# Kernel optimization log

Hardware: AMD Instinct MI355X
Metric: run time of the kernel (lower is better)

## Reference

```python
import jax, jax.numpy as jnp
import numpy as np

B, TH, TS, HS, WS = 16, 1024, 1024, 1024, 1024


def setup_inputs() -> dict:
    key = jax.random.key(0)
    k1, k2, k3, k4 = jax.random.split(key, 4)
    h = jax.random.normal(k1, (B, TH, HS), dtype=jnp.float32)
    s = jax.random.normal(k2, (B, TS, WS), dtype=jnp.float32)
    # nn.Linear params: weight [out, in], bias [out]
    Wh = jax.random.normal(k3, (HS, HS), dtype=jnp.float32) * 0.02
    bh = jnp.zeros((HS,), dtype=jnp.float32)
    Ws = jax.random.normal(k4, (HS, WS), dtype=jnp.float32) * 0.02
    bs = jnp.zeros((HS,), dtype=jnp.float32)
    return {"h": h, "s": s, "Wh": Wh, "bh": bh, "Ws": Ws, "bs": bs}


def reference(h, s, Wh, bh, Ws, bs):
    hp = jnp.einsum('bth,oh->bto', h, Wh) + bh          # [B, TH, HS]
    sp = jnp.einsum('btw,ow->bto', s, Ws) + bs          # [B, TS, HS]
    scores = jnp.einsum('bik,bjk->bij', hp, sp)         # [B, TH, TS]
    b, th, _ = scores.shape
    # faithful to torch: flat-chunk into rows of length TH, softmax over dim 1
    sm = jax.nn.softmax(scores.reshape(-1, th), axis=1).reshape(b, -1, th)  # [B, TS, TH]
    res = jnp.matmul(sm, hp)                            # [B, TS, HS]
    return res.reshape(-1, res.shape[-1])               # [B*TS, HS]
```

## Files before the change

### kernel.cpp

```cpp
#include <hip/hip_runtime.h>
#include <hip/hip_bf16.h>
#include <stdint.h>


typedef _Float16 half_t;
typedef __attribute__((ext_vector_type(8))) _Float16 half8;
typedef __attribute__((ext_vector_type(4))) _Float16 half4;
typedef __attribute__((ext_vector_type(4))) float floatx4;

__device__ __forceinline__ void gl2lds16(const void* g, void* l) {
    __builtin_amdgcn_global_load_lds(
        (const __attribute__((address_space(1))) uint32_t*)(uintptr_t)g,
        (__attribute__((address_space(3))) uint32_t*)(uintptr_t)l,
        16, 0, 0);
}

template<int WH16T>
__global__ __launch_bounds__(256, 4) void gemm128(
    const half_t* __restrict__ A, const half_t* __restrict__ B,
    const float* __restrict__ bias,
    half_t* __restrict__ Ch, half_t* __restrict__ ChT)
{
    __shared__ char smem[32768];

    const int tid  = threadIdx.x;
    const int wave = tid >> 6;
    const int lane = tid & 63;
    const int wr = wave >> 1, wc = wave & 1;
    const int lr = lane & 15, lg = lane >> 4;

    const int row0 = blockIdx.x * 128;
    const int col0 = blockIdx.y * 128;

    floatx4 acc[4][4];
#pragma unroll
    for (int m = 0; m < 4; ++m)
#pragma unroll
        for (int n = 0; n < 4; ++n)
            acc[m][n] = (floatx4){0.f, 0.f, 0.f, 0.f};

    long aOff[2], bOff[2];
#pragma unroll
    for (int i = 0; i < 2; ++i) {
        const int off = i * 4096 + tid * 16;
        const int e = off ^ (((off >> 7) & 3) << 4);
        const int r = e >> 6, cb = e & 63;
        aOff[i] = (long)(row0 + r) * 2048 + cb;
        bOff[i] = (long)(col0 + r) * 2048 + cb;
    }
    const int wave_s = __builtin_amdgcn_readfirstlane(wave);

    auto stage = [&](int buf, int kk) {
#pragma unroll
        for (int i = 0; i < 2; ++i)
            gl2lds16((const char*)A + aOff[i] + (long)kk * 2,
                     smem + buf * 16384 + i * 4096 + wave_s * 1024);
#pragma unroll
        for (int i = 0; i < 2; ++i)
            gl2lds16((const char*)B + bOff[i] + (long)kk * 2,
                     smem + buf * 16384 + 8192 + i * 4096 + wave_s * 1024);
    };

    const uint32_t swx = (uint32_t)((lg * 16) ^ (((lr >> 1) & 3) << 4));
    uint32_t aof = (uint32_t)((wr * 64 + lr) * 64) + swx;
    uint32_t bof = 8192u + (uint32_t)((wc * 64 + lr) * 64) + swx;

    stage(0, 0);
    __syncthreads();

    for (int t = 0; t < 32; ++t) {
        if (t + 1 < 32) stage((t & 1) ^ 1, (t + 1) * 32);

        half8 aF[4], bF[4];
#pragma unroll
        for (int ni = 0; ni < 4; ++ni)
            bF[ni] = *(const half8*)(smem + bof + ni * 1024);
#pragma unroll
        for (int mi = 0; mi < 4; ++mi)
            aF[mi] = *(const half8*)(smem + aof + mi * 1024);
#pragma unroll
        for (int mi = 0; mi < 4; ++mi)
#pragma unroll
            for (int ni = 0; ni < 4; ++ni)
                acc[mi][ni] = __builtin_amdgcn_mfma_f32_16x16x32_f16(
                    aF[mi], bF[ni], acc[mi][ni], 0, 0, 0);

        __syncthreads();
        aof ^= 16384; bof ^= 16384;
    }

    {
        float* wlds = (float*)(smem + wave * 2304);
        float bv[4];
#pragma unroll
        for (int n = 0; n < 4; ++n)
            bv[n] = bias[col0 + wc * 64 + n * 16 + lr];
        const int er = lane >> 2, ec = lane & 3;
        const int oc = lane >> 1, tc = lane & 1;
#pragma unroll
        for (int m = 0; m < 4; ++m) {
#pragma unroll
            for (int np = 0; np < 2; ++np) {
#pragma unroll
                for (int n2 = 0; n2 < 2; ++n2)
#pragma unroll
                    for (int j = 0; j < 4; ++j)
                        wlds[(lg * 4 + j) * 36 + n2 * 16 + lr] =
                            acc[m][np * 2 + n2][j] + bv[np * 2 + n2];
                const int grow = row0 + wr * 64 + m * 16;
                const int gcol = col0 + wc * 64 + np * 32;
                float4 q0 = *(float4*)&wlds[er * 36 + ec * 8];
                float4 q1 = *(float4*)&wlds[er * 36 + ec * 8 + 4];
                {
                    half8 o = { (half_t)q0.x, (half_t)q0.y, (half_t)q0.z, (half_t)q0.w,
                                (half_t)q1.x, (half_t)q1.y, (half_t)q1.z, (half_t)q1.w };
                    *(half8*)&Ch[(long)(grow + er) * 1024 + gcol + ec * 8] = o;
                }
                if (WH16T) {
                    float tv[8];
#pragma unroll
                    for (int k = 0; k < 8; ++k)
                        tv[k] = wlds[(tc * 8 + k) * 36 + oc];
                    half8 o = { (half_t)tv[0], (half_t)tv[1], (half_t)tv[2], (half_t)tv[3],
                                (half_t)tv[4], (half_t)tv[5], (half_t)tv[6], (half_t)tv[7] };
                    const int gt = grow + tc * 8;
                    *(half8*)&ChT[(long)(gt >> 10) * 1048576
                                  + (long)(gcol + oc) * 1024 + (gt & 1023)] = o;
                }
                __builtin_amdgcn_s_waitcnt(0);
            }
        }
    }
}

#define NT16 16

template<int SWZ>
__global__ __launch_bounds__(512, 2) void gemm256(
    const half_t* __restrict__ A, const half_t* __restrict__ B,
    float* __restrict__ Cf,
    int lda, int ldb,
    long aBatch, long bBatch, long cfBatch, int ldcf)
{
    extern __shared__ char smem[];

    const int tid  = threadIdx.x;
    const int wave = tid >> 6;
    const int lane = tid & 63;
    const int wr = wave >> 2;
    const int wc = wave & 3;
    const int lr = lane & 15, lg = lane >> 4;

    long batch; int row0, col0;
    if constexpr (SWZ) {
        const int lin = blockIdx.x + (blockIdx.y << 2) + (blockIdx.z << 4);
        const int xcd = lin & 7, per = lin >> 3;
        batch = (xcd << 1) | (per >> 4);
        const int wt = per & 15;
        row0 = (wt & 3) * 256;
        col0 = (wt >> 2) * 256;
    } else {
        batch = blockIdx.z;
        row0 = blockIdx.x * 256;
        col0 = blockIdx.y * 256;
    }

    const half_t* Ab = A + batch * aBatch;
    const half_t* Bb = B + batch * bBatch;

    floatx4 acc[8][4];
#pragma unroll
    for (int m = 0; m < 8; ++m)
#pragma unroll
        for (int n = 0; n < 4; ++n)
            acc[m][n] = (floatx4){0.f, 0.f, 0.f, 0.f};

    long aOff[2][2], bOff[2][2];
#pragma unroll
    for (int hh = 0; hh < 2; ++hh)
#pragma unroll
        for (int i = 0; i < 2; ++i) {
            const int off = hh * 16384 + i * 8192 + tid * 16;
            const int e = off ^ (((off >> 7) & 7) << 4);
            const int r = e >> 7, cb = e & 127;
            aOff[hh][i] = (long)(row0 + r) * (long)(lda * 2) + cb;
            bOff[hh][i] = (long)(col0 + r) * (long)(ldb * 2) + cb;
        }

    const int wave_s = __builtin_amdgcn_readfirstlane(wave);
    auto stage = [&](int buf, int kk) {
#pragma unroll
        for (int hh = 0; hh < 2; ++hh)
#pragma unroll
            for (int i = 0; i < 2; ++i)
                gl2lds16((const char*)Ab + aOff[hh][i] + (long)kk * 2,
                         smem + buf * 65536 + hh * 16384 + i * 8192 + wave_s * 1024);
#pragma unroll
        for (int hh = 0; hh < 2; ++hh)
#pragma unroll
            for (int i = 0; i < 2; ++i)
                gl2lds16((const char*)Bb + bOff[hh][i] + (long)kk * 2,
                         smem + buf * 65536 + 32768 + hh * 16384 + i * 8192 + wave_s * 1024);
    };

    uint32_t aof0 = (uint32_t)((wr * 128 + lr) * 128 + ((lg * 16) ^ ((lr & 7) << 4)));
    uint32_t aof1 = (uint32_t)((wr * 128 + lr) * 128 + ((64 + lg * 16) ^ ((lr & 7) << 4)));
    uint32_t bof0 = (uint32_t)(32768 + (wc * 64 + lr) * 128 + ((lg * 16) ^ ((lr & 7) << 4)));
    uint32_t bof1 = (uint32_t)(32768 + (wc * 64 + lr) * 128 + ((64 + lg * 16) ^ ((lr & 7) << 4)));

    stage(0, 0);
    __syncthreads();

    for (int t = 0; t < NT16; ++t) {
        if (t + 1 < NT16) stage((t & 1) ^ 1, (t + 1) * 64);

        half8 aF[4][2], bF[4][2];
#pragma unroll
        for (int ni = 0; ni < 4; ++ni) {
            bF[ni][0] = *(const half8*)(smem + bof0 + ni * 2048);
            bF[ni][1] = *(const half8*)(smem + bof1 + ni * 2048);
        }
#pragma unroll
        for (int mi = 0; mi < 4; ++mi) {
            aF[mi][0] = *(const half8*)(smem + aof0 + mi * 2048);
            aF[mi][1] = *(const half8*)(smem + aof1 + mi * 2048);
        }
#pragma unroll
        for (int mi = 0; mi < 4; ++mi)
#pragma unroll
            for (int ni = 0; ni < 4; ++ni)
#pragma unroll
                for (int ks = 0; ks < 2; ++ks)
                    acc[mi][ni] = __builtin_amdgcn_mfma_f32_16x16x32_f16(
                        aF[mi][ks], bF[ni][ks], acc[mi][ni], 0, 0, 0);
#pragma unroll
        for (int mi = 0; mi < 4; ++mi) {
            aF[mi][0] = *(const half8*)(smem + aof0 + (4 + mi) * 2048);
            aF[mi][1] = *(const half8*)(smem + aof1 + (4 + mi) * 2048);
        }
#pragma unroll
        for (int mi = 0; mi < 4; ++mi)
#pragma unroll
            for (int ni = 0; ni < 4; ++ni)
#pragma unroll
                for (int ks = 0; ks < 2; ++ks)
                    acc[4 + mi][ni] = __builtin_amdgcn_mfma_f32_16x16x32_f16(
                        aF[mi][ks], bF[ni][ks], acc[4 + mi][ni], 0, 0, 0);

        __syncthreads();
        aof0 ^= 65536; aof1 ^= 65536; bof0 ^= 65536; bof1 ^= 65536;
    }

    {
        float* wlds = (float*)(smem + wave * 2304);
        const int er = lane >> 2, ec = lane & 3;
#pragma unroll
        for (int m = 0; m < 8; ++m) {
#pragma unroll
            for (int np = 0; np < 2; ++np) {
#pragma unroll
                for (int n2 = 0; n2 < 2; ++n2)
#pragma unroll
                    for (int j = 0; j < 4; ++j)
                        wlds[(lg * 4 + j) * 36 + n2 * 16 + lr] = acc[m][np * 2 + n2][j];
                const int grow = row0 + wr * 128 + m * 16;
                const int gcol = col0 + wc * 64 + np * 32;
                float4 q0 = *(float4*)&wlds[er * 36 + ec * 8];
                float4 q1 = *(float4*)&wlds[er * 36 + ec * 8 + 4];
                float* p = Cf + batch * cfBatch + (long)(grow + er) * ldcf + gcol + ec * 8;
                *(float4*)p = q0;
                *(float4*)(p + 4) = q1;
                __builtin_amdgcn_s_waitcnt(0);
            }
        }
    }
}

__global__ void softmax_inplace(float* __restrict__ S) {
    const long r = blockIdx.x;
    float* row = S + r * 1024;
    const int tid = threadIdx.x;
    const int wave = tid >> 6, lane = tid & 63;

    float4 v = ((const float4*)row)[tid];
    float mx = fmaxf(fmaxf(v.x, v.y), fmaxf(v.z, v.w));
#pragma unroll
    for (int off = 32; off > 0; off >>= 1)
        mx = fmaxf(mx, __shfl_xor(mx, off));
    __shared__ float rmx[4], rsm[4];
    if (lane == 0) rmx[wave] = mx;
    __syncthreads();
    mx = fmaxf(fmaxf(rmx[0], rmx[1]), fmaxf(rmx[2], rmx[3]));

    float e0 = __expf(v.x - mx), e1 = __expf(v.y - mx);
    float e2 = __expf(v.z - mx), e3 = __expf(v.w - mx);
    float s = e0 + e1 + e2 + e3;
#pragma unroll
    for (int off = 32; off > 0; off >>= 1)
        s += __shfl_xor(s, off);
    if (lane == 0) rsm[wave] = s;
    __syncthreads();
    s = rsm[0] + rsm[1] + rsm[2] + rsm[3];

    const float inv = 1.0f / s;
    half4 o = { (half_t)(e0 * inv), (half_t)(e1 * inv), (half_t)(e2 * inv), (half_t)(e3 * inv) };
    ((half4*)((half_t*)S + r * 2048))[tid] = o;
}

__global__ void cvt_f16(const float4* __restrict__ src, half4* __restrict__ dst, int n4) {
    const int stride = gridDim.x * blockDim.x;
    for (int i = blockIdx.x * blockDim.x + threadIdx.x; i < n4; i += stride) {
        float4 v = src[i];
        half4 o = { (half_t)v.x, (half_t)v.y, (half_t)v.z, (half_t)v.w };
        dst[i] = o;
    }
}

extern "C" void kernel_launch(void* const* d_in, const int* in_sizes, int n_in,
                              void* d_out, int out_size, void* d_ws, size_t ws_size,
                              hipStream_t stream) {
    const float* h  = (const float*)d_in[0];
    const float* s  = (const float*)d_in[1];
    const float* Wh = (const float*)d_in[2];
    const float* bh = (const float*)d_in[3];
    const float* Ws = (const float*)d_in[4];
    const float* bs = (const float*)d_in[5];

    const long MB = 16384;
    const long D  = 1024;

    char* w = (char*)d_ws;
    float*  sc   = (float*)w;   w += MB * D * 4;
    half_t* Wh16 = (half_t*)w;  w += D * D * 2;
    half_t* Ws16 = (half_t*)w;  w += D * D * 2;
    half_t* h16  = (half_t*)w;  w += MB * D * 2;
    half_t* s16  = (half_t*)w;  w += MB * D * 2;
    half_t* hp16 = (half_t*)w;  w += MB * D * 2;
    half_t* sp16 = (half_t*)w;  w += MB * D * 2;
    half_t* hpT  = (half_t*)w;  w += MB * D * 2;

    (void)hipFuncSetAttribute(reinterpret_cast<const void*>(&gemm256<1>),
                        hipFuncAttributeMaxDynamicSharedMemorySize, 131072);

    cvt_f16<<<512,  256, 0, stream>>>((const float4*)Wh, (half4*)Wh16, (int)(D * D / 4));
    cvt_f16<<<512,  256, 0, stream>>>((const float4*)Ws, (half4*)Ws16, (int)(D * D / 4));
    cvt_f16<<<2048, 256, 0, stream>>>((const float4*)h,  (half4*)h16,  (int)(MB * D / 4));
    cvt_f16<<<2048, 256, 0, stream>>>((const float4*)s,  (half4*)s16,  (int)(MB * D / 4));

    gemm128<1><<<dim3(128, 8), 256, 0, stream>>>(h16, Wh16, bh, hp16, hpT);
    gemm128<0><<<dim3(128, 8), 256, 0, stream>>>(s16, Ws16, bs, sp16, nullptr);
    gemm256<1><<<dim3(4, 4, 16), 512, 131072, stream>>>(
        hp16, sp16, sc, 1024, 1024, 1048576L, 1048576L, 1048576L, 1024);
    softmax_inplace<<<16384, 256, 0, stream>>>(sc);
    gemm256<1><<<dim3(4, 4, 16), 512, 131072, stream>>>(
        (const half_t*)sc, hpT, (float*)d_out, 2048, 1024,
        2097152L, 1048576L, 1048576L, 1024);
}
```

Before: 247.8 us.

## Fuse fp32-to-fp16 activation conversion into projection GEMM and merge both projections

The projection GEMM now loads the fp32 activations h and s straight into LDS and converts them to fp16 while building the MFMA fragments. This removes the two large standalone conversion kernels and their fp16 intermediate buffers. The h and s projections also run in one launch, selected by blockIdx.z. In exchange each A tile now takes twice the global bandwidth and twice the LDS, occupancy drops to 3 blocks per CU, and the conversion work moves into the GEMM inner loop.

New measurement: 249.2 us. No clear change (+0.6%).

```diff
diff --git a/kernel.cpp b/kernel.cpp
--- a/kernel.cpp
+++ b/kernel.cpp
@@ -15,13 +15,14 @@
         16, 0, 0);
 }
 
-template<int WH16T>
-__global__ __launch_bounds__(256, 4) void gemm128(
-    const half_t* __restrict__ A, const half_t* __restrict__ B,
-    const float* __restrict__ bias,
-    half_t* __restrict__ Ch, half_t* __restrict__ ChT)
+__global__ __launch_bounds__(256, 3) void gemm128f(
+    const float* __restrict__ Ah, const float* __restrict__ As,
+    const half_t* __restrict__ Wha, const half_t* __restrict__ Wsa,
+    const float* __restrict__ bha, const float* __restrict__ bsa,
+    half_t* __restrict__ hp, half_t* __restrict__ sp,
+    half_t* __restrict__ hpT)
 {
-    __shared__ char smem[32768];
+    __shared__ char smem[49152];
 
     const int tid  = threadIdx.x;
     const int wave = tid >> 6;
@@ -29,6 +30,13 @@
     const int wr = wave >> 1, wc = wave & 1;
     const int lr = lane & 15, lg = lane >> 4;
 
+    const int z = blockIdx.z;
+    const float*  A32  = z ? As  : Ah;
+    const half_t* Bw   = z ? Wsa : Wha;
+    const float*  bias = z ? bsa : bha;
+    half_t*       Ch   = z ? sp  : hp;
+    const int doT = (z == 0);
+
     const int row0 = blockIdx.x * 128;
     const int col0 = blockIdx.y * 128;
 
@@ -39,31 +47,41 @@
         for (int n = 0; n < 4; ++n)
             acc[m][n] = (floatx4){0.f, 0.f, 0.f, 0.f};
 
-    long aOff[2], bOff[2];
+    long aOff[4], bOff[2];
+#pragma unroll
+    for (int c = 0; c < 4; ++c) {
+        const int off = c * 4096 + tid * 16;
+        const int e = off ^ (((off >> 7) & 7) << 4);
+        const int r = e >> 7, cb = e & 127;
+        aOff[c] = (long)(row0 + r) * 4096 + cb;
+    }
 #pragma unroll
     for (int i = 0; i < 2; ++i) {
         const int off = i * 4096 + tid * 16;
         const int e = off ^ (((off >> 7) & 3) << 4);
         const int r = e >> 6, cb = e & 63;
-        aOff[i] = (long)(row0 + r) * 2048 + cb;
         bOff[i] = (long)(col0 + r) * 2048 + cb;
     }
     const int wave_s = __builtin_amdgcn_readfirstlane(wave);
 
     auto stage = [&](int buf, int kk) {
 #pragma unroll
+        for (int c = 0; c < 4; ++c)
+            gl2lds16((const char*)A32 + aOff[c] + (long)kk * 4,
+                     smem + buf * 24576 + c * 4096 + wave_s * 1024);
+#pragma unroll
         for (int i = 0; i < 2; ++i)
-            gl2lds16((const char*)A + aOff[i] + (long)kk * 2,
-                     smem + buf * 16384 + i * 4096 + wave_s * 1024);
-#pragma unroll
-        for (int i = 0; i < 2; ++i)
-            gl2lds16((const char*)B + bOff[i] + (long)kk * 2,
-                     smem + buf * 16384 + 8192 + i * 4096 + wave_s * 1024);
+            gl2lds16((const char*)Bw + bOff[i] + (long)kk * 2,
+                     smem + buf * 24576 + 16384 + i * 4096 + wave_s * 1024);
     };
 
-    const uint32_t swx = (uint32_t)((lg * 16) ^ (((lr >> 1) & 3) << 4));
-    uint32_t aof = (uint32_t)((wr * 64 + lr) * 64) + swx;
-    uint32_t bof = 8192u + (uint32_t)((wc * 64 + lr) * 64) + swx;
+    uint32_t aofu[2];
+#pragma unroll
+    for (int u = 0; u < 2; ++u)
+        aofu[u] = (uint32_t)((wr * 64 + lr) * 128
+                             + ((lg * 32 + u * 16) ^ ((lr & 7) << 4)));
+    const uint32_t bof = 16384u + (uint32_t)((wc * 64 + lr) * 64
+                             + ((lg * 16) ^ (((lr >> 1) & 3) << 4)));
 
     stage(0, 0);
     __syncthreads();
@@ -71,13 +89,19 @@
     for (int t = 0; t < 32; ++t) {
         if (t + 1 < 32) stage((t & 1) ^ 1, (t + 1) * 32);
 
+        const uint32_t bb = (uint32_t)(t & 1) * 24576u;
+
         half8 aF[4], bF[4];
 #pragma unroll
         for (int ni = 0; ni < 4; ++ni)
-            bF[ni] = *(const half8*)(smem + bof + ni * 1024);
-#pragma unroll
-        for (int mi = 0; mi < 4; ++mi)
-            aF[mi] = *(const half8*)(smem + aof + mi * 1024);
+            bF[ni] = *(const half8*)(smem + bb + bof + ni * 1024);
+#pragma unroll
+        for (int mi = 0; mi < 4; ++mi) {
+            float4 p = *(const float4*)(smem + bb + aofu[0] + mi * 2048);
+            float4 q = *(const float4*)(smem + bb + aofu[1] + mi * 2048);
+            aF[mi] = (half8){ (half_t)p.x, (half_t)p.y, (half_t)p.z, (half_t)p.w,
+                              (half_t)q.x, (half_t)q.y, (half_t)q.z, (half_t)q.w };
+        }
 #pragma unroll
         for (int mi = 0; mi < 4; ++mi)
 #pragma unroll
@@ -86,7 +110,6 @@
                     aF[mi], bF[ni], acc[mi][ni], 0, 0, 0);
 
         __syncthreads();
-        aof ^= 16384; bof ^= 16384;
     }
 
     {
@@ -116,7 +139,7 @@
                                 (half_t)q1.x, (half_t)q1.y, (half_t)q1.z, (half_t)q1.w };
                     *(half8*)&Ch[(long)(grow + er) * 1024 + gcol + ec * 8] = o;
                 }
-                if (WH16T) {
+                if (doT) {
                     float tv[8];
 #pragma unroll
                     for (int k = 0; k < 8; ++k)
@@ -124,7 +147,7 @@
                     half8 o = { (half_t)tv[0], (half_t)tv[1], (half_t)tv[2], (half_t)tv[3],
                                 (half_t)tv[4], (half_t)tv[5], (half_t)tv[6], (half_t)tv[7] };
                     const int gt = grow + tc * 8;
-                    *(half8*)&ChT[(long)(gt >> 10) * 1048576
+                    *(half8*)&hpT[(long)(gt >> 10) * 1048576
                                   + (long)(gcol + oc) * 1024 + (gt & 1023)] = o;
                 }
                 __builtin_amdgcn_s_waitcnt(0);
@@ -333,8 +356,6 @@
     float*  sc   = (float*)w;   w += MB * D * 4;
     half_t* Wh16 = (half_t*)w;  w += D * D * 2;
     half_t* Ws16 = (half_t*)w;  w += D * D * 2;
-    half_t* h16  = (half_t*)w;  w += MB * D * 2;
-    half_t* s16  = (half_t*)w;  w += MB * D * 2;
     half_t* hp16 = (half_t*)w;  w += MB * D * 2;
     half_t* sp16 = (half_t*)w;  w += MB * D * 2;
     half_t* hpT  = (half_t*)w;  w += MB * D * 2;
@@ -342,13 +363,11 @@
     (void)hipFuncSetAttribute(reinterpret_cast<const void*>(&gemm256<1>),
                         hipFuncAttributeMaxDynamicSharedMemorySize, 131072);
 
-    cvt_f16<<<512,  256, 0, stream>>>((const float4*)Wh, (half4*)Wh16, (int)(D * D / 4));
-    cvt_f16<<<512,  256, 0, stream>>>((const float4*)Ws, (half4*)Ws16, (int)(D * D / 4));
-    cvt_f16<<<2048, 256, 0, stream>>>((const float4*)h,  (half4*)h16,  (int)(MB * D / 4));
-    cvt_f16<<<2048, 256, 0, stream>>>((const float4*)s,  (half4*)s16,  (int)(MB * D / 4));
-
-    gemm128<1><<<dim3(128, 8), 256, 0, stream>>>(h16, Wh16, bh, hp16, hpT);
-    gemm128<0><<<dim3(128, 8), 256, 0, stream>>>(s16, Ws16, bs, sp16, nullptr);
+    cvt_f16<<<512, 256, 0, stream>>>((const float4*)Wh, (half4*)Wh16, (int)(D * D / 4));
+    cvt_f16<<<512, 256, 0, stream>>>((const float4*)Ws, (half4*)Ws16, (int)(D * D / 4));
+
+    gemm128f<<<dim3(128, 8, 2), 256, 0, stream>>>(
+        h, s, Wh16, Ws16, bh, bs, hp16, sp16, hpT);
     gemm256<1><<<dim3(4, 4, 16), 512, 131072, stream>>>(
         hp16, sp16, sc, 1024, 1024, 1048576L, 1048576L, 1048576L, 1024);
     softmax_inplace<<<16384, 256, 0, stream>>>(sc);
```
